# Kernel tuning notes

Measured on AMD Instinct MI355X. Metric: run time of the kernel, lower is better.

Reference implementation:

```python
import jax, jax.numpy as jnp
import numpy as np

HIDDEN = 16
N_CLASSES = 10
N_NODES = 100000
N_EDGES = 3200000
D_FEAT = 128
NEG_SLOPE = 0.1


def setup_inputs() -> dict:
    key = jax.random.key(0)
    k1, k2, k3 = jax.random.split(key, 3)
    features = jax.random.normal(k1, (N_NODES, D_FEAT), dtype=jnp.float32)
    edge_src = jax.random.randint(k2, (N_EDGES,), 0, N_NODES, dtype=jnp.int64)
    edge_dst = jax.random.randint(k3, (N_EDGES,), 0, N_NODES, dtype=jnp.int64)
    return {"features": features, "edge_src": edge_src, "edge_dst": edge_dst}


def reference(features, edge_src, edge_dst):
    # SpMM: h[v] = sum over edges (u->v) of features[u]   (binary adjacency)
    msgs = features[edge_src]                      # [E, F] irregular gather
    h = jax.ops.segment_sum(msgs, edge_dst, num_segments=N_NODES)  # [N, F]
    # x @ ones(F, HIDDEN): every column equals the row-sum of h
    r1 = jnp.sum(h, axis=-1)                       # [N]
    a1 = jax.nn.leaky_relu(r1, NEG_SLOPE)          # leaky relu, slope 0.1
    # x @ ones(HIDDEN, N_CLASSES): each class column = HIDDEN * a1
    r2 = HIDDEN * a1
    a2 = jax.nn.leaky_relu(r2, NEG_SLOPE)
    # x @ ones(N_CLASSES, 1) then .int() and flatten
    r3 = N_CLASSES * a2                            # [N]
    return r3.astype(jnp.int32).reshape(-1)
```

## Files before the change

### kernel.cpp

```cpp
#include <hip/hip_runtime.h>

#define N_NODES  100000
#define N_EDGES  3200000
#define D_FEAT   128
#define SLICE    20000
#define SLICE4   (SLICE / 4)
#define N_SLICES 5
#define NCHUNK   80
#define EPB      40000
#define EPT      8
#define TPB      1024
#define STRIDE   (TPB * EPT)

__device__ __forceinline__ unsigned short f2bf(float f) {
    union { float f; unsigned u; } c; c.f = f;
    unsigned r = c.u + 0x7FFFu + ((c.u >> 16) & 1u);
    return (unsigned short)(r >> 16);
}
__device__ __forceinline__ float bf2f(unsigned short h) {
    union { unsigned u; float f; } c; c.u = ((unsigned)h) << 16; return c.f;
}

__global__ void __launch_bounds__(256) rowsum_kernel(
    const float* __restrict__ feat,
    float* __restrict__ rowsum)
{
    const int gid = (int)(blockIdx.x * blockDim.x + threadIdx.x);
    const int row = gid >> 5;
    const int sub = gid & 31;
    if (row >= N_NODES) return;

    const float4 v = reinterpret_cast<const float4*>(
        feat + (size_t)row * D_FEAT)[sub];
    float s = (v.x + v.y) + (v.z + v.w);

    #pragma unroll
    for (int off = 16; off > 0; off >>= 1)
        s += __shfl_xor(s, off, 64);

    if (sub == 0) rowsum[row] = s;
}

__global__ void __launch_bounds__(TPB, 8) scatter_kernel(
    const int* __restrict__ edge_src,
    const int* __restrict__ edge_dst,
    const float* __restrict__ rowsum,
    unsigned short* __restrict__ copies)
{
    __shared__ float lds[SLICE];

    const int tid = (int)threadIdx.x;
    const int bid = (int)blockIdx.x;
    const int g   = bid / 40;
    const int r   = bid % 40;
    const int xcd = r & 7;
    const int s   = r >> 3;
    const int b   = g * 8 + xcd;
    const int lo  = s * SLICE;

    float4 z; z.x = z.y = z.z = z.w = 0.0f;
    for (int i = tid; i < SLICE4; i += TPB)
        reinterpret_cast<float4*>(lds)[i] = z;
    __syncthreads();

    const int begin = b * EPB;
    const int end   = begin + EPB;

    int e = begin + tid * EPT;
    bool v = (e < end);

    int4 d0, d1, s0, s1;
    if (v) {
        d0 = *(const int4*)(edge_dst + e);     s0 = *(const int4*)(edge_src + e);
        d1 = *(const int4*)(edge_dst + e + 4); s1 = *(const int4*)(edge_src + e + 4);
    }

    while (v) {
        const int en = e + STRIDE;
        const bool vn = (en < end);
        int4 nd0, nd1, ns0, ns1;
        if (vn) {
            nd0 = *(const int4*)(edge_dst + en);     ns0 = *(const int4*)(edge_src + en);
            nd1 = *(const int4*)(edge_dst + en + 4); ns1 = *(const int4*)(edge_src + en + 4);
        }

        const unsigned j0 = (unsigned)(d0.x - lo);
        const unsigned j1 = (unsigned)(d0.y - lo);
        const unsigned j2 = (unsigned)(d0.z - lo);
        const unsigned j3 = (unsigned)(d0.w - lo);
        const unsigned j4 = (unsigned)(d1.x - lo);
        const unsigned j5 = (unsigned)(d1.y - lo);
        const unsigned j6 = (unsigned)(d1.z - lo);
        const unsigned j7 = (unsigned)(d1.w - lo);

        float w0 = (j0 < SLICE) ? rowsum[s0.x] : 0.0f;
        float w1 = (j1 < SLICE) ? rowsum[s0.y] : 0.0f;
        float w2 = (j2 < SLICE) ? rowsum[s0.z] : 0.0f;
        float w3 = (j3 < SLICE) ? rowsum[s0.w] : 0.0f;
        float w4 = (j4 < SLICE) ? rowsum[s1.x] : 0.0f;
        float w5 = (j5 < SLICE) ? rowsum[s1.y] : 0.0f;
        float w6 = (j6 < SLICE) ? rowsum[s1.z] : 0.0f;
        float w7 = (j7 < SLICE) ? rowsum[s1.w] : 0.0f;

        if (j0 < SLICE) atomicAdd(&lds[j0], w0);
        if (j1 < SLICE) atomicAdd(&lds[j1], w1);
        if (j2 < SLICE) atomicAdd(&lds[j2], w2);
        if (j3 < SLICE) atomicAdd(&lds[j3], w3);
        if (j4 < SLICE) atomicAdd(&lds[j4], w4);
        if (j5 < SLICE) atomicAdd(&lds[j5], w5);
        if (j6 < SLICE) atomicAdd(&lds[j6], w6);
        if (j7 < SLICE) atomicAdd(&lds[j7], w7);

        e = en; v = vn;
        d0 = nd0; d1 = nd1; s0 = ns0; s1 = ns1;
    }
    __syncthreads();

    unsigned short* __restrict__ dstp = copies + ((size_t)s * NCHUNK + b) * SLICE;
    for (int i = tid; i < SLICE4; i += TPB) {
        const float4 vv = reinterpret_cast<const float4*>(lds)[i];
        ushort4 o;
        o.x = f2bf(vv.x); o.y = f2bf(vv.y); o.z = f2bf(vv.z); o.w = f2bf(vv.w);
        reinterpret_cast<ushort4*>(dstp)[i] = o;
    }
}

__global__ void __launch_bounds__(256) reduce_final_kernel(
    const unsigned short* __restrict__ copies,
    int* __restrict__ out)
{
    const int i4 = (int)(blockIdx.x * blockDim.x + threadIdx.x);
    if (i4 >= N_NODES / 4) return;

    const int s  = i4 / SLICE4;
    const int j4 = i4 - s * SLICE4;

    float ax = 0.0f, ay = 0.0f, az = 0.0f, aw = 0.0f;
    const ushort4* base = reinterpret_cast<const ushort4*>(copies)
                        + (size_t)s * NCHUNK * SLICE4 + j4;
    #pragma unroll 4
    for (int c = 0; c < NCHUNK; ++c) {
        const ushort4 v = base[(size_t)c * SLICE4];
        ax += bf2f(v.x); ay += bf2f(v.y); az += bf2f(v.z); aw += bf2f(v.w);
    }

    auto act = [](float x) -> int {
        const float a1 = (x  > 0.0f) ? x  : 0.1f * x;
        const float r2 = 16.0f * a1;
        const float a2 = (r2 > 0.0f) ? r2 : 0.1f * r2;
        return (int)(10.0f * a2);
    };

    int4 o;
    o.x = act(ax); o.y = act(ay); o.z = act(az); o.w = act(aw);
    reinterpret_cast<int4*>(out)[i4] = o;
}

extern "C" void kernel_launch(void* const* d_in, const int* in_sizes, int n_in,
                              void* d_out, int out_size, void* d_ws, size_t ws_size,
                              hipStream_t stream)
{
    const float* feat     = (const float*)d_in[0];
    const int*   edge_src = (const int*)d_in[1];
    const int*   edge_dst = (const int*)d_in[2];
    int*         out      = (int*)d_out;

    float* rowsum = (float*)d_ws;
    unsigned short* copies = (unsigned short*)(rowsum + N_NODES);

    {
        const int threads = 256;
        const long long total = (long long)N_NODES * 32;
        const int blocks = (int)((total + threads - 1) / threads);
        rowsum_kernel<<<blocks, threads, 0, stream>>>(feat, rowsum);
    }

    scatter_kernel<<<N_SLICES * NCHUNK, TPB, 0, stream>>>(edge_src, edge_dst,
                                                          rowsum, copies);

    {
        const int threads = 256;
        const int blocks = (N_NODES / 4 + threads - 1) / threads;
        reduce_final_kernel<<<blocks, threads, 0, stream>>>(copies, out);
    }
}
```

Measured before the change: 52.17 us.

## Split edge gather into separate bf16 pass and use three wider LDS slices

Adds a gather kernel that looks up rowsum[src] once per edge and stores it as bf16. The scatter kernel then streams dst indices and the precomputed bf16 values instead of gathering rowsum for every slice. The node range is now cut into 3 slices of about 33K floats in LDS rather than 5, so each edge's dst index is read fewer times. The cost is an extra kernel launch, extra 6.4 MB of global write/read traffic, bf16 rounding of per-edge values, and larger LDS per block, which can lower occupancy.

```diff
diff --git a/kernel.cpp b/kernel.cpp
--- a/kernel.cpp
+++ b/kernel.cpp
@@ -3,14 +3,13 @@
 #define N_NODES  100000
 #define N_EDGES  3200000
 #define D_FEAT   128
-#define SLICE    20000
+#define SLICE    33344
 #define SLICE4   (SLICE / 4)
-#define N_SLICES 5
+#define N_SLICES 3
 #define NCHUNK   80
 #define EPB      40000
-#define EPT      8
 #define TPB      1024
-#define STRIDE   (TPB * EPT)
+#define STRIDE   (TPB * 8)
 
 __device__ __forceinline__ unsigned short f2bf(float f) {
     union { float f; unsigned u; } c; c.f = f;
@@ -41,22 +40,37 @@
     if (sub == 0) rowsum[row] = s;
 }
 
-__global__ void __launch_bounds__(TPB, 8) scatter_kernel(
+__global__ void __launch_bounds__(256) gather_kernel(
     const int* __restrict__ edge_src,
+    const float* __restrict__ rowsum,
+    unsigned short* __restrict__ val)
+{
+    const int e = ((int)(blockIdx.x * 256 + threadIdx.x)) * 4;
+    const int4 s4 = *reinterpret_cast<const int4*>(edge_src + e);
+    ushort4 o;
+    o.x = f2bf(rowsum[s4.x]);
+    o.y = f2bf(rowsum[s4.y]);
+    o.z = f2bf(rowsum[s4.z]);
+    o.w = f2bf(rowsum[s4.w]);
+    *reinterpret_cast<ushort4*>(val + e) = o;
+}
+
+__global__ void __launch_bounds__(TPB) scatter2_kernel(
     const int* __restrict__ edge_dst,
-    const float* __restrict__ rowsum,
+    const unsigned short* __restrict__ val,
     unsigned short* __restrict__ copies)
 {
     __shared__ float lds[SLICE];
 
     const int tid = (int)threadIdx.x;
     const int bid = (int)blockIdx.x;
-    const int g   = bid / 40;
-    const int r   = bid % 40;
+    const int g   = bid / 24;
+    const int r   = bid % 24;
     const int xcd = r & 7;
     const int s   = r >> 3;
     const int b   = g * 8 + xcd;
     const int lo  = s * SLICE;
+    const unsigned len = (unsigned)((N_NODES - lo < SLICE) ? (N_NODES - lo) : SLICE);
 
     float4 z; z.x = z.y = z.z = z.w = 0.0f;
     for (int i = tid; i < SLICE4; i += TPB)
@@ -66,22 +80,28 @@
     const int begin = b * EPB;
     const int end   = begin + EPB;
 
-    int e = begin + tid * EPT;
+    int e = begin + tid * 8;
     bool v = (e < end);
 
-    int4 d0, d1, s0, s1;
+    int4    d0, d1;
+    ushort4 w01;
+    ushort4 w23;
     if (v) {
-        d0 = *(const int4*)(edge_dst + e);     s0 = *(const int4*)(edge_src + e);
-        d1 = *(const int4*)(edge_dst + e + 4); s1 = *(const int4*)(edge_src + e + 4);
+        d0  = *(const int4*)(edge_dst + e);
+        d1  = *(const int4*)(edge_dst + e + 4);
+        w01 = *(const ushort4*)(val + e);
+        w23 = *(const ushort4*)(val + e + 4);
     }
 
     while (v) {
         const int en = e + STRIDE;
         const bool vn = (en < end);
-        int4 nd0, nd1, ns0, ns1;
+        int4 nd0, nd1; ushort4 nw01, nw23;
         if (vn) {
-            nd0 = *(const int4*)(edge_dst + en);     ns0 = *(const int4*)(edge_src + en);
-            nd1 = *(const int4*)(edge_dst + en + 4); ns1 = *(const int4*)(edge_src + en + 4);
+            nd0  = *(const int4*)(edge_dst + en);
+            nd1  = *(const int4*)(edge_dst + en + 4);
+            nw01 = *(const ushort4*)(val + en);
+            nw23 = *(const ushort4*)(val + en + 4);
         }
 
         const unsigned j0 = (unsigned)(d0.x - lo);
@@ -93,31 +113,23 @@
         const unsigned j6 = (unsigned)(d1.z - lo);
         const unsigned j7 = (unsigned)(d1.w - lo);
 
-        float w0 = (j0 < SLICE) ? rowsum[s0.x] : 0.0f;
-        float w1 = (j1 < SLICE) ? rowsum[s0.y] : 0.0f;
-        float w2 = (j2 < SLICE) ? rowsum[s0.z] : 0.0f;
-        float w3 = (j3 < SLICE) ? rowsum[s0.w] : 0.0f;
-        float w4 = (j4 < SLICE) ? rowsum[s1.x] : 0.0f;
-        float w5 = (j5 < SLICE) ? rowsum[s1.y] : 0.0f;
-        float w6 = (j6 < SLICE) ? rowsum[s1.z] : 0.0f;
-        float w7 = (j7 < SLICE) ? rowsum[s1.w] : 0.0f;
-
-        if (j0 < SLICE) atomicAdd(&lds[j0], w0);
-        if (j1 < SLICE) atomicAdd(&lds[j1], w1);
-        if (j2 < SLICE) atomicAdd(&lds[j2], w2);
-        if (j3 < SLICE) atomicAdd(&lds[j3], w3);
-        if (j4 < SLICE) atomicAdd(&lds[j4], w4);
-        if (j5 < SLICE) atomicAdd(&lds[j5], w5);
-        if (j6 < SLICE) atomicAdd(&lds[j6], w6);
-        if (j7 < SLICE) atomicAdd(&lds[j7], w7);
+        if (j0 < len) atomicAdd(&lds[j0], bf2f(w01.x));
+        if (j1 < len) atomicAdd(&lds[j1], bf2f(w01.y));
+        if (j2 < len) atomicAdd(&lds[j2], bf2f(w01.z));
+        if (j3 < len) atomicAdd(&lds[j3], bf2f(w01.w));
+        if (j4 < len) atomicAdd(&lds[j4], bf2f(w23.x));
+        if (j5 < len) atomicAdd(&lds[j5], bf2f(w23.y));
+        if (j6 < len) atomicAdd(&lds[j6], bf2f(w23.z));
+        if (j7 < len) atomicAdd(&lds[j7], bf2f(w23.w));
 
         e = en; v = vn;
-        d0 = nd0; d1 = nd1; s0 = ns0; s1 = ns1;
+        d0 = nd0; d1 = nd1; w01 = nw01; w23 = nw23;
     }
     __syncthreads();
 
     unsigned short* __restrict__ dstp = copies + ((size_t)s * NCHUNK + b) * SLICE;
-    for (int i = tid; i < SLICE4; i += TPB) {
+    const int len4 = (int)len >> 2;
+    for (int i = tid; i < len4; i += TPB) {
         const float4 vv = reinterpret_cast<const float4*>(lds)[i];
         ushort4 o;
         o.x = f2bf(vv.x); o.y = f2bf(vv.y); o.z = f2bf(vv.z); o.w = f2bf(vv.w);
@@ -132,7 +144,7 @@
     const int i4 = (int)(blockIdx.x * blockDim.x + threadIdx.x);
     if (i4 >= N_NODES / 4) return;
 
-    const int s  = i4 / SLICE4;
+    const int s  = (i4 >= 2 * SLICE4) ? 2 : (i4 >= SLICE4 ? 1 : 0);
     const int j4 = i4 - s * SLICE4;
 
     float ax = 0.0f, ay = 0.0f, az = 0.0f, aw = 0.0f;
@@ -165,8 +177,9 @@
     const int*   edge_dst = (const int*)d_in[2];
     int*         out      = (int*)d_out;
 
-    float* rowsum = (float*)d_ws;
-    unsigned short* copies = (unsigned short*)(rowsum + N_NODES);
+    float* rowsum          = (float*)d_ws;
+    unsigned short* val    = (unsigned short*)(rowsum + N_NODES);
+    unsigned short* copies = val + N_EDGES;
 
     {
         const int threads = 256;
@@ -175,8 +188,9 @@
         rowsum_kernel<<<blocks, threads, 0, stream>>>(feat, rowsum);
     }
 
-    scatter_kernel<<<N_SLICES * NCHUNK, TPB, 0, stream>>>(edge_src, edge_dst,
-                                                          rowsum, copies);
+    gather_kernel<<<N_EDGES / (256 * 4), 256, 0, stream>>>(edge_src, rowsum, val);
+
+    scatter2_kernel<<<N_SLICES * NCHUNK, TPB, 0, stream>>>(edge_dst, val, copies);
 
     {
         const int threads = 256;
```

Measured after the change: 61.30 us. 17.5% more time.
